# Kernel optimization log

Hardware: AMD Instinct MI355X
Metric: run time of the kernel (lower is better)

Reference implementation:

```python
import jax, jax.numpy as jnp
import numpy as np

B, S, IN, EMB, H = 4, 2048, 256, 512, 8
D = EMB // H
SCALE = 1.0 / np.sqrt(EMB)  # source uses 1/sqrt(embed_size), not head_dim
EPS = 1e-5


def setup_inputs() -> dict:
    key = jax.random.key(0)
    ks = jax.random.split(key, 20)
    def w(k, shape, fan_in):
        return jax.random.normal(k, shape, jnp.float32) * (1.0 / np.sqrt(fan_in))
    inp = {"state_emb": jax.random.normal(ks[0], (B, S, IN), jnp.float32)}
    i = 1
    for p in ("q", "k", "v"):
        inp[f"{p}_W1"] = w(ks[i], (IN, EMB), IN); i += 1
        inp[f"{p}_b1"] = jnp.zeros((EMB,), jnp.float32)
        inp[f"{p}_W2"] = w(ks[i], (EMB, EMB), EMB); i += 1
        inp[f"{p}_b2"] = jnp.zeros((EMB,), jnp.float32)
    inp["f_W1"] = w(ks[i], (EMB, 2 * EMB), EMB); i += 1
    inp["f_b1"] = jnp.zeros((2 * EMB,), jnp.float32)
    inp["f_W2"] = w(ks[i], (2 * EMB, EMB), 2 * EMB); i += 1
    inp["f_b2"] = jnp.zeros((EMB,), jnp.float32)
    inp["ln1_g"] = jnp.ones((EMB,), jnp.float32)
    inp["ln1_b"] = jnp.zeros((EMB,), jnp.float32)
    inp["ln2_g"] = jnp.ones((EMB,), jnp.float32)
    inp["ln2_b"] = jnp.zeros((EMB,), jnp.float32)
    return inp


def _mlp2(x, W1, b1, W2, b2):
    return jax.nn.relu(x @ W1 + b1) @ W2 + b2


def _layernorm(x, g, b):
    mu = jnp.mean(x, axis=-1, keepdims=True)
    var = jnp.mean(jnp.square(x - mu), axis=-1, keepdims=True)
    return (x - mu) * jax.lax.rsqrt(var + EPS) * g + b


def reference(state_emb, q_W1, q_b1, q_W2, q_b2, k_W1, k_b1, k_W2, k_b2,
              v_W1, v_b1, v_W2, v_b2, f_W1, f_b1, f_W2, f_b2,
              ln1_g, ln1_b, ln2_g, ln2_b):
    n, dim = state_emb.shape[0], state_emb.shape[1]
    q = _mlp2(state_emb, q_W1, q_b1, q_W2, q_b2)  # [n, dim, EMB]
    k = _mlp2(state_emb, k_W1, k_b1, k_W2, k_b2)
    v = _mlp2(state_emb, v_W1, v_b1, v_W2, v_b2)
    qh = q.reshape(n, dim, H, D)
    kh = k.reshape(n, dim, H, D)
    vh = v.reshape(n, dim, H, D)
    energy = jnp.einsum('nqhd,nkhd->nhqk', qh, kh)  # [n, H, dim, dim]
    attn = jax.nn.softmax(energy * SCALE, axis=-1)
    ctx = jnp.einsum('nhql,nlhd->nqhd', attn, vh).reshape(n, dim, EMB)
    x = _layernorm(ctx + q, ln1_g, ln1_b)  # residual with queries, per source
    ff = _mlp2(x, f_W1, f_b1, f_W2, f_b2)
    return _layernorm(x + ff, ln2_g, ln2_b)
```

## Files before the change

kernel.cpp:

```cpp
#include <hip/hip_runtime.h>
#include <hip/hip_bf16.h>
#include <math.h>

#define BB   4
#define SS   2048
#define INF_ 256
#define EMB  512
#define NH   8
#define HD   64
#define NT   8192

typedef unsigned short u16;
typedef unsigned int   u32;
typedef __attribute__((ext_vector_type(8))) short bf16x8;
typedef __attribute__((ext_vector_type(8))) unsigned short u16x8;
typedef __attribute__((ext_vector_type(4))) float f32x4;

constexpr float C2  = 0.06375871607f;
constexpr float RB  = 0.005624549f;
constexpr float TB  = 1.00390625f;
constexpr float EPS = 1e-5f;

__device__ __forceinline__ u16 f2bf(float v) {
    __hip_bfloat16 h = __float2bfloat16(v);
    return *(u16*)&h;
}
__device__ __forceinline__ float bf2f(u16 u) {
    __hip_bfloat16 h = *(__hip_bfloat16*)&u;
    return __bfloat162float(h);
}
__device__ __forceinline__ u16 ftrunc_bf(float v) {
    return (u16)(__float_as_uint(v * TB) >> 16);
}
__device__ __forceinline__ f32x4 mfma16(bf16x8 a, bf16x8 b, f32x4 c) {
    return __builtin_amdgcn_mfma_f32_16x16x32_bf16(a, b, c, 0, 0, 0);
}
__device__ __forceinline__ void async16(const void* g, void* l) {
    __builtin_amdgcn_global_load_lds(
        (const __attribute__((address_space(1))) void*)g,
        (__attribute__((address_space(3))) void*)l, 16, 0, 0);
}
__device__ __forceinline__ int derive_flag(const u16* x) {
    const int lane = threadIdx.x & 63;
    const unsigned e = (x[lane * 2] >> 7) & 0xFF;
    float pl = (e == 0 || (e >= 110 && e <= 140)) ? 1.0f : 0.0f;
    #pragma unroll
    for (int o = 1; o < 64; o <<= 1) pl += __shfl_xor(pl, o);
    return pl < 32.0f;
}

__global__ __launch_bounds__(256) void prep(
    const u16* __restrict__ xsrc,
    const void* w0, const void* w1, const void* w2, const void* w3,
    const void* w4, const void* w5, const void* w6, const void* w7,
    const void* p0, const void* p1, const void* p2, const void* p3,
    const void* p4, const void* p5, const void* p6, const void* p7,
    const void* p8, const void* p9, const void* p10, const void* p11,
    u16* __restrict__ xbf, u16* __restrict__ wt1, u16* __restrict__ wt2,
    u16* __restrict__ f1t, u16* __restrict__ f2t, float* __restrict__ small)
{
    const int isf = derive_flag(xsrc);
    const int z = blockIdx.z;
    const int tid = threadIdx.x;

    if (z < 8) {
        int K, M; const void* src; u16* dst;
        switch (z) {
            case 0: K=256;  M=512;  src=w0; dst=wt1;             break;
            case 1: K=256;  M=512;  src=w1; dst=wt1+512*256;     break;
            case 2: K=256;  M=512;  src=w2; dst=wt1+2*512*256;   break;
            case 3: K=512;  M=512;  src=w3; dst=wt2;             break;
            case 4: K=512;  M=512;  src=w4; dst=wt2+512*512;     break;
            case 5: K=512;  M=512;  src=w5; dst=wt2+2*512*512;   break;
            case 6: K=512;  M=1024; src=w6; dst=f1t;             break;
            default:K=1024; M=512;  src=w7; dst=f2t;             break;
        }
        const int m0 = blockIdx.x * 32, k0 = blockIdx.y * 32;
        if (m0 >= M || k0 >= K) return;
        __shared__ u16 t[32][33];
        const int tx = tid & 31, ty = tid >> 5;
        #pragma unroll
        for (int i = 0; i < 4; ++i) {
            const int kk = k0 + ty + i * 8;
            t[ty + i * 8][tx] = isf ? ftrunc_bf(((const float*)src)[(size_t)kk * M + m0 + tx])
                                    : ((const u16*)src)[(size_t)kk * M + m0 + tx];
        }
        __syncthreads();
        #pragma unroll
        for (int i = 0; i < 4; ++i) {
            const int mm = m0 + ty + i * 8;
            dst[(size_t)mm * K + k0 + tx] = t[tx][ty + i * 8];
        }
    } else if (z == 8) {
        const int bid = blockIdx.y * 32 + blockIdx.x;
        const int base = bid * 2048 + tid * 8;
        if (isf) {
            #pragma unroll
            for (int j = 0; j < 8; ++j)
                xbf[base + j] = ftrunc_bf(((const float*)xsrc)[base + j]);
        } else {
            *(u16x8*)&xbf[base] = *(const u16x8*)&xsrc[base];
        }
    } else {
        const int bid = blockIdx.y * 32 + blockIdx.x;
        if (bid >= 28) return;
        const int e = bid * 256 + tid;
        int id, i;
        if (e < 3072)      { id = e >> 9;               i = e & 511;          }
        else if (e < 4096) { id = 6;                    i = e - 3072;         }
        else               { id = 7 + ((e - 4096) >> 9); i = (e - 4096) & 511; }
        const void* src;
        switch (id) {
            case 0: src = p0; break;  case 1: src = p1; break;
            case 2: src = p2; break;  case 3: src = p3; break;
            case 4: src = p4; break;  case 5: src = p5; break;
            case 6: src = p6; break;  case 7: src = p7; break;
            case 8: src = p8; break;  case 9: src = p9; break;
            case 10: src = p10; break; default: src = p11; break;
        }
        small[e] = isf ? ((const float*)src)[i] : bf2f(((const u16*)src)[i]);
    }
}

template <int TR, int TC, bool RELU, bool AWHICH, bool VOUT>
__global__ __launch_bounds__(256) void gemm_bt(
    const u16* __restrict__ Aall, const u16* __restrict__ Wtall,
    const float* __restrict__ ball, u16* __restrict__ out,
    u16* __restrict__ vtb, int N, int K, int M)
{
    constexpr int RT = TR / 32, CT = TC / 32;
    constexpr int AR = TR / 32, BR = TC / 32;
    constexpr int SSTAGE = (TR + TC) * 64;
    constexpr int SELEMS = VOUT ? (SSTAGE > 128 * 136 ? SSTAGE : 128 * 136) : SSTAGE;
    __shared__ __align__(16) u16 smem[SELEMS];
    u16* sA = smem;
    u16* sB = smem + TR * 64;

    const int mtiles = M / TC;
    const int which = blockIdx.x / mtiles;
    const int colb  = blockIdx.x % mtiles;
    const int row0 = blockIdx.y * TR, col0 = colb * TC;
    const u16* A  = Aall + (AWHICH ? (size_t)which * N * K : 0);
    const u16* Wt = Wtall + (size_t)which * M * K;
    const float* bias = ball + (size_t)which * M;

    const int tid = threadIdx.x;
    const int lane = tid & 63, w = tid >> 6;
    const int wrow = (w & 1) * (TR / 2), wcol = (w >> 1) * (TC / 2);
    const int c = lane & 15, quad = lane >> 4;

    const u16* ap[AR]; const u16* bp[BR];
    #pragma unroll
    for (int i = 0; i < AR; ++i) {
        const int raw = i * 256 + tid, r = raw >> 3, ch = (raw & 7) ^ (r & 7);
        ap[i] = A + (size_t)(row0 + r) * K + ch * 8;
    }
    #pragma unroll
    for (int i = 0; i < BR; ++i) {
        const int raw = i * 256 + tid, r = raw >> 3, ch = (raw & 7) ^ (r & 7);
        bp[i] = Wt + (size_t)(col0 + r) * K + ch * 8;
    }

    f32x4 acc[RT][CT] = {};

    for (int k0 = 0; k0 < K; k0 += 64) {
        __syncthreads();
        #pragma unroll
        for (int i = 0; i < AR; ++i) {
            async16(ap[i], (char*)sA + (i * 256 + tid) * 16);
            ap[i] += 64;
        }
        #pragma unroll
        for (int i = 0; i < BR; ++i) {
            async16(bp[i], (char*)sB + (i * 256 + tid) * 16);
            bp[i] += 64;
        }
        __syncthreads();

        #pragma unroll
        for (int kt = 0; kt < 2; ++kt) {
            bf16x8 af[RT], bfr[CT];
            #pragma unroll
            for (int rt = 0; rt < RT; ++rt) {
                const int r = wrow + rt * 16 + c;
                af[rt] = *(const bf16x8*)&sA[(r * 8 + ((kt * 4 + quad) ^ (r & 7))) * 8];
            }
            #pragma unroll
            for (int ct = 0; ct < CT; ++ct) {
                const int r = wcol + ct * 16 + c;
                bfr[ct] = *(const bf16x8*)&sB[(r * 8 + ((kt * 4 + quad) ^ (r & 7))) * 8];
            }
            #pragma unroll
            for (int rt = 0; rt < RT; ++rt)
                #pragma unroll
                for (int ct = 0; ct < CT; ++ct)
                    acc[rt][ct] = mfma16(af[rt], bfr[ct], acc[rt][ct]);
        }
    }

    if (VOUT && which == 2) {
        __syncthreads();
        #pragma unroll
        for (int rt = 0; rt < RT; ++rt) {
            const int rowb = wrow + rt * 16 + quad * 4;
            #pragma unroll
            for (int ct = 0; ct < CT; ++ct) {
                const int col = wcol + ct * 16 + c;
                ushort4 pk;
                pk.x = ftrunc_bf(acc[rt][ct][0] + bias[col0 + col]);
                pk.y = ftrunc_bf(acc[rt][ct][1] + bias[col0 + col]);
                pk.z = ftrunc_bf(acc[rt][ct][2] + bias[col0 + col]);
                pk.w = ftrunc_bf(acc[rt][ct][3] + bias[col0 + col]);
                *(ushort4*)&smem[col * 136 + rowb] = pk;
            }
        }
        __syncthreads();
        const int dl = tid >> 1, half = tid & 1;
        const int hg = (col0 + dl) >> 6, dd = (col0 + dl) & 63;
        const int bb = row0 >> 11, s0 = row0 & 2047;
        u16* dst = vtb + ((size_t)(bb * NH + hg) * HD + dd) * SS + s0 + half * 64;
        #pragma unroll
        for (int j = 0; j < 8; ++j)
            *(u16x8*)&dst[j * 8] = *(const u16x8*)&smem[dl * 136 + half * 64 + j * 8];
        return;
    }

    const size_t outW = (size_t)which * N * M;
    #pragma unroll
    for (int rt = 0; rt < RT; ++rt) {
        #pragma unroll
        for (int i = 0; i < 4; ++i) {
            const int row = row0 + wrow + rt * 16 + quad * 4 + i;
            #pragma unroll
            for (int ct = 0; ct < CT; ++ct) {
                const int col = col0 + wcol + ct * 16 + c;
                float v = acc[rt][ct][i] + bias[col];
                if (RELU) v = fmaxf(v, 0.0f);
                out[outW + (size_t)row * M + col] = ftrunc_bf(v);
            }
        }
    }
}

__global__ __launch_bounds__(256) void attn_mfma(
    const u16* __restrict__ q, const u16* __restrict__ k,
    const u16* __restrict__ vt, u16* __restrict__ ctx)
{
    __shared__ __align__(16) u16 sK[2][64 * 64];
    __shared__ __align__(16) u16 sV[2][64 * 64];
    __shared__ __align__(16) u16 sP[4][32 * 64];

    const int tid = threadIdx.x;
    const int w = tid >> 6, lane = tid & 63;
    const int c = lane & 15, quad = lane >> 4;
    const int id = blockIdx.x;
    const int slot = id >> 3;
    const int bh = ((id & 7) << 2) | (slot >> 4);
    const int qt = slot & 15;
    const int b = bh >> 3, h = bh & 7;
    const int q0 = qt * 128;
    const size_t tokbase = (size_t)b * SS;
    const int hoff = h * HD;

    bf16x8 qf[2][2];
    #pragma unroll
    for (int f = 0; f < 2; ++f)
        #pragma unroll
        for (int kt = 0; kt < 2; ++kt)
            qf[f][kt] = *(const bf16x8*)&q[(tokbase + q0 + w * 32 + f * 16 + c) * EMB
                                           + hoff + kt * 32 + quad * 8];

    const u16* kp[2]; const u16* vp[2];
    #pragma unroll
    for (int i = 0; i < 2; ++i) {
        const int raw = i * 256 + tid, rr = raw >> 3, ch = (raw & 7) ^ (rr & 7);
        kp[i] = k + (tokbase + rr) * EMB + hoff + ch * 8;
        vp[i] = vt + ((size_t)(b * NH + h) * HD + rr) * SS + ch * 8;
    }
    auto stage = [&](int buf) {
        #pragma unroll
        for (int i = 0; i < 2; ++i) {
            async16(kp[i], (char*)sK[buf] + (i * 256 + tid) * 16);
            kp[i] += 64 * EMB;
        }
        #pragma unroll
        for (int i = 0; i < 2; ++i) {
            async16(vp[i], (char*)sV[buf] + (i * 256 + tid) * 16);
            vp[i] += 64;
        }
    };
    stage(0);

    float l0 = 0.0f, l1 = 0.0f;
    f32x4 accO[2][4] = {};

    for (int t = 0; t < SS / 64; ++t) {
        __syncthreads();
        const int buf = t & 1;
        if (t < SS / 64 - 1) stage(buf ^ 1);

        f32x4 accS[2][4] = {};
        #pragma unroll
        for (int mt = 0; mt < 4; ++mt) {
            const int key = mt * 16 + c;
            #pragma unroll
            for (int kt = 0; kt < 2; ++kt) {
                bf16x8 kf = *(const bf16x8*)&sK[buf][(key * 8 + ((kt * 4 + quad) ^ (key & 7))) * 8];
                accS[0][mt] = mfma16(kf, qf[0][kt], accS[0][mt]);
                accS[1][mt] = mfma16(kf, qf[1][kt], accS[1][mt]);
            }
        }

        #pragma unroll
        for (int f = 0; f < 2; ++f) {
            const int row = f * 16 + c;
            float ls = 0.0f;
            u32 pw[8];
            #pragma unroll
            for (int mt = 0; mt < 4; ++mt) {
                const float e0 = __builtin_amdgcn_exp2f(fmaf(accS[f][mt][0], C2, RB));
                const float e1 = __builtin_amdgcn_exp2f(fmaf(accS[f][mt][1], C2, RB));
                const float e2 = __builtin_amdgcn_exp2f(fmaf(accS[f][mt][2], C2, RB));
                const float e3 = __builtin_amdgcn_exp2f(fmaf(accS[f][mt][3], C2, RB));
                ls += (e0 + e1) + (e2 + e3);
                pw[2 * mt]     = __builtin_amdgcn_perm(__float_as_uint(e1), __float_as_uint(e0), 0x07060302u);
                pw[2 * mt + 1] = __builtin_amdgcn_perm(__float_as_uint(e3), __float_as_uint(e2), 0x07060302u);
            }
            if (f == 0) l0 += ls; else l1 += ls;
            #pragma unroll
            for (int mt = 0; mt < 4; ++mt) {
                const int chunk = 2 * mt + (quad >> 1);
                uint2 u; u.x = pw[2 * mt]; u.y = pw[2 * mt + 1];
                *(uint2*)((char*)&sP[w][0] + (row * 8 + (chunk ^ (c & 7))) * 16 + 8 * (quad & 1)) = u;
            }
        }

        bf16x8 pf[2][2];
        #pragma unroll
        for (int f = 0; f < 2; ++f)
            #pragma unroll
            for (int kt = 0; kt < 2; ++kt)
                pf[f][kt] = *(const bf16x8*)&sP[w][((f * 16 + c) * 8 + ((kt * 4 + quad) ^ (c & 7))) * 8];
        #pragma unroll
        for (int nt = 0; nt < 4; ++nt) {
            const int d = nt * 16 + c;
            #pragma unroll
            for (int kt = 0; kt < 2; ++kt) {
                bf16x8 vf = *(const bf16x8*)&sV[buf][(d * 8 + ((kt * 4 + quad) ^ (d & 7))) * 8];
                accO[0][nt] = mfma16(pf[0][kt], vf, accO[0][nt]);
                accO[1][nt] = mfma16(pf[1][kt], vf, accO[1][nt]);
            }
        }
    }

    #pragma unroll
    for (int f = 0; f < 2; ++f) {
        float l = (f == 0) ? l0 : l1;
        l += __shfl_xor(l, 16);
        l += __shfl_xor(l, 32);
        float li[4];
        #pragma unroll
        for (int i = 0; i < 4; ++i) {
            const float lv = __shfl(l, quad * 4 + i, 16);
            li[i] = (lv > 0.0f) ? (1.0f / lv) : 0.0f;
        }
        #pragma unroll
        for (int nt = 0; nt < 4; ++nt)
            #pragma unroll
            for (int i = 0; i < 4; ++i) {
                const int tok = q0 + w * 32 + f * 16 + quad * 4 + i;
                ctx[(tokbase + tok) * EMB + hoff + nt * 16 + c] =
                    ftrunc_bf(accO[f][nt][i] * li[i]);
            }
    }
}

__global__ __launch_bounds__(256) void ln_mid(
    const u16* __restrict__ a, const u16* __restrict__ b2,
    const float* __restrict__ g, const float* __restrict__ be,
    u16* __restrict__ outb)
{
    const int wave = threadIdx.x >> 6, lane = threadIdx.x & 63;
    const size_t row = (size_t)blockIdx.x * 4 + wave;
    const u16x8 av = *(const u16x8*)&a[row * EMB + lane * 8];
    const u16x8 bv = *(const u16x8*)&b2[row * EMB + lane * 8];
    float vals[8], sum = 0.0f;
    #pragma unroll
    for (int i = 0; i < 8; ++i) { vals[i] = bf2f(av[i]) + bf2f(bv[i]); sum += vals[i]; }
    #pragma unroll
    for (int o = 1; o < 64; o <<= 1) sum += __shfl_xor(sum, o);
    const float mu = sum * (1.0f / 512.0f);
    float vs = 0.0f;
    #pragma unroll
    for (int i = 0; i < 8; ++i) { const float d = vals[i] - mu; vs += d * d; }
    #pragma unroll
    for (int o = 1; o < 64; o <<= 1) vs += __shfl_xor(vs, o);
    const float rstd = rsqrtf(vs * (1.0f / 512.0f) + EPS);
    u16x8 ov;
    #pragma unroll
    for (int i = 0; i < 8; ++i) {
        const int col = lane * 8 + i;
        ov[i] = f2bf((vals[i] - mu) * rstd * g[col] + be[col]);
    }
    *(u16x8*)&outb[row * EMB + lane * 8] = ov;
}

__global__ __launch_bounds__(256) void ln_final(
    const u16* __restrict__ a, const u16* __restrict__ b2,
    const float* __restrict__ g, const float* __restrict__ be,
    void* __restrict__ dout, const u16* __restrict__ xsrc)
{
    const int isf = derive_flag(xsrc);
    const int wave = threadIdx.x >> 6, lane = threadIdx.x & 63;
    const size_t row = (size_t)blockIdx.x * 4 + wave;
    const u16x8 av = *(const u16x8*)&a[row * EMB + lane * 8];
    const u16x8 bv = *(const u16x8*)&b2[row * EMB + lane * 8];
    float vals[8], sum = 0.0f;
    #pragma unroll
    for (int i = 0; i < 8; ++i) { vals[i] = bf2f(av[i]) + bf2f(bv[i]); sum += vals[i]; }
    #pragma unroll
    for (int o = 1; o < 64; o <<= 1) sum += __shfl_xor(sum, o);
    const float mu = sum * (1.0f / 512.0f);
    float vs = 0.0f;
    #pragma unroll
    for (int i = 0; i < 8; ++i) { const float d = vals[i] - mu; vs += d * d; }
    #pragma unroll
    for (int o = 1; o < 64; o <<= 1) vs += __shfl_xor(vs, o);
    const float rstd = rsqrtf(vs * (1.0f / 512.0f) + EPS);
    if (isf) {
        #pragma unroll
        for (int i = 0; i < 8; ++i) {
            const int col = lane * 8 + i;
            ((float*)dout)[row * EMB + col] = (vals[i] - mu) * rstd * g[col] + be[col];
        }
    } else {
        u16x8 ov;
        #pragma unroll
        for (int i = 0; i < 8; ++i) {
            const int col = lane * 8 + i;
            ov[i] = f2bf((vals[i] - mu) * rstd * g[col] + be[col]);
        }
        *(u16x8*)&((u16*)dout)[row * EMB + lane * 8] = ov;
    }
}

extern "C" void kernel_launch(void* const* d_in, const int* in_sizes, int n_in,
                              void* d_out, int out_size, void* d_ws, size_t ws_size,
                              hipStream_t stream)
{
    char* ws = (char*)d_ws;
    float* small = (float*)(ws + 0);
    u16*   wt1   = (u16*)(ws + 32768);
    u16*   wt2   = (u16*)(ws + 819200);
    u16*   f1t   = (u16*)(ws + 2392064);
    u16*   f2t   = (u16*)(ws + 3440640);
    u16*   xbf   = (u16*)(ws + 4489216);
    u16*   h3    = (u16*)(ws + 8683520);
    u16*   qkv   = (u16*)(ws + 33849344);
    u16*   vtb   = (u16*)(ws + 59015168);
    u16*   ctxb  = (u16*)(ws + 67403776);
    u16*   x1b   = (u16*)(ws + 75792384);
    u16*   ffb   = (u16*)(ws + 84180992);

    const dim3 blk(256);
    const u16* xsrc = (const u16*)d_in[0];

    prep<<<dim3(32, 32, 10), blk, 0, stream>>>(
        xsrc,
        d_in[1], d_in[5], d_in[9], d_in[3], d_in[7], d_in[11], d_in[13], d_in[15],
        d_in[2], d_in[6], d_in[10], d_in[4], d_in[8], d_in[12],
        d_in[14], d_in[16], d_in[17], d_in[18], d_in[19], d_in[20],
        xbf, wt1, wt2, f1t, f2t, small);

    gemm_bt<128, 128, true, false, false><<<dim3(12, 64), blk, 0, stream>>>(
        xbf, wt1, small + 0, h3, nullptr, NT, INF_, EMB);
    gemm_bt<128, 128, false, true, true><<<dim3(12, 64), blk, 0, stream>>>(
        h3, wt2, small + 1536, qkv, vtb, NT, EMB, EMB);

    attn_mfma<<<dim3(512), blk, 0, stream>>>(
        qkv, qkv + (size_t)NT * EMB, vtb, ctxb);

    ln_mid<<<NT / 4, blk, 0, stream>>>(ctxb, qkv, small + 4608, small + 5120, x1b);

    u16* h2 = h3;
    gemm_bt<128, 128, true, false, false><<<dim3(8, 64), blk, 0, stream>>>(
        x1b, f1t, small + 3072, h2, nullptr, NT, EMB, 1024);
    gemm_bt<128, 64, false, false, false><<<dim3(8, 64), blk, 0, stream>>>(
        h2, f2t, small + 4096, ffb, nullptr, NT, 1024, EMB);

    ln_final<<<NT / 4, blk, 0, stream>>>(x1b, ffb, small + 5632, small + 6144, d_out, xsrc);
}
```

Baseline: 260.6 us.

## Double-buffer GEMM tiles, shrink attention query tile, pass P via bpermute

The GEMM kernel now double-buffers its A/B shared-memory tiles. It prefetches the next K-slice with async copies while computing the current one, which removes one barrier per iteration. The attention kernel drops to 64 queries per block (16 per wave) and is launched on twice as many blocks. Probabilities move from the S MFMA output layout to the PV operand layout with ds_bpermute instead of a shared-memory round trip. The QKV and FFN1 GEMMs switch to 128x64 tiles with twice the grid, trading some reuse for occupancy and parallelism.

```diff
diff --git a/kernel.cpp b/kernel.cpp
--- a/kernel.cpp
+++ b/kernel.cpp
@@ -130,11 +130,8 @@
 {
     constexpr int RT = TR / 32, CT = TC / 32;
     constexpr int AR = TR / 32, BR = TC / 32;
-    constexpr int SSTAGE = (TR + TC) * 64;
-    constexpr int SELEMS = VOUT ? (SSTAGE > 128 * 136 ? SSTAGE : 128 * 136) : SSTAGE;
-    __shared__ __align__(16) u16 smem[SELEMS];
-    u16* sA = smem;
-    u16* sB = smem + TR * 64;
+    __shared__ __align__(16) u16 sA[2][TR * 64];
+    __shared__ __align__(16) u16 sB[2][TC * 64];
 
     const int mtiles = M / TC;
     const int which = blockIdx.x / mtiles;
@@ -160,22 +157,27 @@
         const int raw = i * 256 + tid, r = raw >> 3, ch = (raw & 7) ^ (r & 7);
         bp[i] = Wt + (size_t)(col0 + r) * K + ch * 8;
     }
+    auto stage = [&](int buf) {
+        #pragma unroll
+        for (int i = 0; i < AR; ++i) {
+            async16(ap[i], (char*)&sA[buf][0] + (i * 256 + tid) * 16);
+            ap[i] += 64;
+        }
+        #pragma unroll
+        for (int i = 0; i < BR; ++i) {
+            async16(bp[i], (char*)&sB[buf][0] + (i * 256 + tid) * 16);
+            bp[i] += 64;
+        }
+    };
+    stage(0);
 
     f32x4 acc[RT][CT] = {};
-
-    for (int k0 = 0; k0 < K; k0 += 64) {
+    const int nIter = K >> 6;
+
+    for (int t = 0; t < nIter; ++t) {
         __syncthreads();
-        #pragma unroll
-        for (int i = 0; i < AR; ++i) {
-            async16(ap[i], (char*)sA + (i * 256 + tid) * 16);
-            ap[i] += 64;
-        }
-        #pragma unroll
-        for (int i = 0; i < BR; ++i) {
-            async16(bp[i], (char*)sB + (i * 256 + tid) * 16);
-            bp[i] += 64;
-        }
-        __syncthreads();
+        const int buf = t & 1;
+        if (t + 1 < nIter) stage(buf ^ 1);
 
         #pragma unroll
         for (int kt = 0; kt < 2; ++kt) {
@@ -183,12 +185,12 @@
             #pragma unroll
             for (int rt = 0; rt < RT; ++rt) {
                 const int r = wrow + rt * 16 + c;
-                af[rt] = *(const bf16x8*)&sA[(r * 8 + ((kt * 4 + quad) ^ (r & 7))) * 8];
+                af[rt] = *(const bf16x8*)&sA[buf][(r * 8 + ((kt * 4 + quad) ^ (r & 7))) * 8];
             }
             #pragma unroll
             for (int ct = 0; ct < CT; ++ct) {
                 const int r = wcol + ct * 16 + c;
-                bfr[ct] = *(const bf16x8*)&sB[(r * 8 + ((kt * 4 + quad) ^ (r & 7))) * 8];
+                bfr[ct] = *(const bf16x8*)&sB[buf][(r * 8 + ((kt * 4 + quad) ^ (r & 7))) * 8];
             }
             #pragma unroll
             for (int rt = 0; rt < RT; ++rt)
@@ -199,6 +201,7 @@
     }
 
     if (VOUT && which == 2) {
+        u16* smem = &sA[0][0];
         __syncthreads();
         #pragma unroll
         for (int rt = 0; rt < RT; ++rt) {
@@ -206,22 +209,23 @@
             #pragma unroll
             for (int ct = 0; ct < CT; ++ct) {
                 const int col = wcol + ct * 16 + c;
+                const float bb = bias[col0 + col];
                 ushort4 pk;
-                pk.x = ftrunc_bf(acc[rt][ct][0] + bias[col0 + col]);
-                pk.y = ftrunc_bf(acc[rt][ct][1] + bias[col0 + col]);
-                pk.z = ftrunc_bf(acc[rt][ct][2] + bias[col0 + col]);
-                pk.w = ftrunc_bf(acc[rt][ct][3] + bias[col0 + col]);
+                pk.x = ftrunc_bf(acc[rt][ct][0] + bb);
+                pk.y = ftrunc_bf(acc[rt][ct][1] + bb);
+                pk.z = ftrunc_bf(acc[rt][ct][2] + bb);
+                pk.w = ftrunc_bf(acc[rt][ct][3] + bb);
                 *(ushort4*)&smem[col * 136 + rowb] = pk;
             }
         }
         __syncthreads();
-        const int dl = tid >> 1, half = tid & 1;
-        const int hg = (col0 + dl) >> 6, dd = (col0 + dl) & 63;
+        const int dcol = tid >> 2, part = tid & 3;
+        const int hg = (col0 + dcol) >> 6, dd = (col0 + dcol) & 63;
         const int bb = row0 >> 11, s0 = row0 & 2047;
-        u16* dst = vtb + ((size_t)(bb * NH + hg) * HD + dd) * SS + s0 + half * 64;
-        #pragma unroll
-        for (int j = 0; j < 8; ++j)
-            *(u16x8*)&dst[j * 8] = *(const u16x8*)&smem[dl * 136 + half * 64 + j * 8];
+        u16* dst = vtb + ((size_t)(bb * NH + hg) * HD + dd) * SS + s0 + part * 32;
+        #pragma unroll
+        for (int j = 0; j < 4; ++j)
+            *(u16x8*)&dst[j * 8] = *(const u16x8*)&smem[dcol * 136 + part * 32 + j * 8];
         return;
     }
 
@@ -248,27 +252,24 @@
 {
     __shared__ __align__(16) u16 sK[2][64 * 64];
     __shared__ __align__(16) u16 sV[2][64 * 64];
-    __shared__ __align__(16) u16 sP[4][32 * 64];
 
     const int tid = threadIdx.x;
     const int w = tid >> 6, lane = tid & 63;
     const int c = lane & 15, quad = lane >> 4;
     const int id = blockIdx.x;
     const int slot = id >> 3;
-    const int bh = ((id & 7) << 2) | (slot >> 4);
-    const int qt = slot & 15;
+    const int bh = ((id & 7) << 2) | (slot >> 5);
+    const int qt = slot & 31;
     const int b = bh >> 3, h = bh & 7;
-    const int q0 = qt * 128;
+    const int q0 = qt * 64;
     const size_t tokbase = (size_t)b * SS;
     const int hoff = h * HD;
 
-    bf16x8 qf[2][2];
-    #pragma unroll
-    for (int f = 0; f < 2; ++f)
-        #pragma unroll
-        for (int kt = 0; kt < 2; ++kt)
-            qf[f][kt] = *(const bf16x8*)&q[(tokbase + q0 + w * 32 + f * 16 + c) * EMB
-                                           + hoff + kt * 32 + quad * 8];
+    const int myq = q0 + w * 16 + c;
+    bf16x8 qf[2];
+    #pragma unroll
+    for (int kt = 0; kt < 2; ++kt)
+        qf[kt] = *(const bf16x8*)&q[(tokbase + myq) * EMB + hoff + kt * 32 + quad * 8];
 
     const u16* kp[2]; const u16* vp[2];
     #pragma unroll
@@ -280,98 +281,85 @@
     auto stage = [&](int buf) {
         #pragma unroll
         for (int i = 0; i < 2; ++i) {
-            async16(kp[i], (char*)sK[buf] + (i * 256 + tid) * 16);
+            async16(kp[i], (char*)&sK[buf][0] + (i * 256 + tid) * 16);
             kp[i] += 64 * EMB;
         }
         #pragma unroll
         for (int i = 0; i < 2; ++i) {
-            async16(vp[i], (char*)sV[buf] + (i * 256 + tid) * 16);
+            async16(vp[i], (char*)&sV[buf][0] + (i * 256 + tid) * 16);
             vp[i] += 64;
         }
     };
     stage(0);
 
-    float l0 = 0.0f, l1 = 0.0f;
-    f32x4 accO[2][4] = {};
+    const int addr0 = (c + 16 * ((quad & 1) * 2)) * 4;
+    const int addr1 = addr0 + 64;
+
+    float l_lane = 0.0f;
+    f32x4 accO[4] = {};
 
     for (int t = 0; t < SS / 64; ++t) {
         __syncthreads();
         const int buf = t & 1;
-        if (t < SS / 64 - 1) stage(buf ^ 1);
-
-        f32x4 accS[2][4] = {};
+        if (t + 1 < SS / 64) stage(buf ^ 1);
+
+        f32x4 accS[4] = {};
         #pragma unroll
         for (int mt = 0; mt < 4; ++mt) {
             const int key = mt * 16 + c;
             #pragma unroll
             for (int kt = 0; kt < 2; ++kt) {
                 bf16x8 kf = *(const bf16x8*)&sK[buf][(key * 8 + ((kt * 4 + quad) ^ (key & 7))) * 8];
-                accS[0][mt] = mfma16(kf, qf[0][kt], accS[0][mt]);
-                accS[1][mt] = mfma16(kf, qf[1][kt], accS[1][mt]);
-            }
-        }
-
-        #pragma unroll
-        for (int f = 0; f < 2; ++f) {
-            const int row = f * 16 + c;
-            float ls = 0.0f;
-            u32 pw[8];
-            #pragma unroll
-            for (int mt = 0; mt < 4; ++mt) {
-                const float e0 = __builtin_amdgcn_exp2f(fmaf(accS[f][mt][0], C2, RB));
-                const float e1 = __builtin_amdgcn_exp2f(fmaf(accS[f][mt][1], C2, RB));
-                const float e2 = __builtin_amdgcn_exp2f(fmaf(accS[f][mt][2], C2, RB));
-                const float e3 = __builtin_amdgcn_exp2f(fmaf(accS[f][mt][3], C2, RB));
-                ls += (e0 + e1) + (e2 + e3);
-                pw[2 * mt]     = __builtin_amdgcn_perm(__float_as_uint(e1), __float_as_uint(e0), 0x07060302u);
-                pw[2 * mt + 1] = __builtin_amdgcn_perm(__float_as_uint(e3), __float_as_uint(e2), 0x07060302u);
-            }
-            if (f == 0) l0 += ls; else l1 += ls;
-            #pragma unroll
-            for (int mt = 0; mt < 4; ++mt) {
-                const int chunk = 2 * mt + (quad >> 1);
-                uint2 u; u.x = pw[2 * mt]; u.y = pw[2 * mt + 1];
-                *(uint2*)((char*)&sP[w][0] + (row * 8 + (chunk ^ (c & 7))) * 16 + 8 * (quad & 1)) = u;
-            }
-        }
-
-        bf16x8 pf[2][2];
-        #pragma unroll
-        for (int f = 0; f < 2; ++f)
-            #pragma unroll
-            for (int kt = 0; kt < 2; ++kt)
-                pf[f][kt] = *(const bf16x8*)&sP[w][((f * 16 + c) * 8 + ((kt * 4 + quad) ^ (c & 7))) * 8];
-        #pragma unroll
-        for (int nt = 0; nt < 4; ++nt) {
-            const int d = nt * 16 + c;
-            #pragma unroll
-            for (int kt = 0; kt < 2; ++kt) {
+                accS[mt] = mfma16(kf, qf[kt], accS[mt]);
+            }
+        }
+
+        u32 pw[8];
+        float ls = 0.0f;
+        #pragma unroll
+        for (int mt = 0; mt < 4; ++mt) {
+            const float e0 = __builtin_amdgcn_exp2f(fmaf(accS[mt][0], C2, RB));
+            const float e1 = __builtin_amdgcn_exp2f(fmaf(accS[mt][1], C2, RB));
+            const float e2 = __builtin_amdgcn_exp2f(fmaf(accS[mt][2], C2, RB));
+            const float e3 = __builtin_amdgcn_exp2f(fmaf(accS[mt][3], C2, RB));
+            ls += (e0 + e1) + (e2 + e3);
+            pw[2 * mt]     = __builtin_amdgcn_perm(__float_as_uint(e1), __float_as_uint(e0), 0x07060302u);
+            pw[2 * mt + 1] = __builtin_amdgcn_perm(__float_as_uint(e3), __float_as_uint(e2), 0x07060302u);
+        }
+        l_lane += ls;
+
+        #pragma unroll
+        for (int kt = 0; kt < 2; ++kt) {
+            const int m = (quad >> 1) + 2 * kt;
+            union { u32 u[4]; bf16x8 v; } pb;
+            pb.u[0] = (u32)__builtin_amdgcn_ds_bpermute(addr0, (int)pw[2 * m]);
+            pb.u[1] = (u32)__builtin_amdgcn_ds_bpermute(addr0, (int)pw[2 * m + 1]);
+            pb.u[2] = (u32)__builtin_amdgcn_ds_bpermute(addr1, (int)pw[2 * m]);
+            pb.u[3] = (u32)__builtin_amdgcn_ds_bpermute(addr1, (int)pw[2 * m + 1]);
+            #pragma unroll
+            for (int nt = 0; nt < 4; ++nt) {
+                const int d = nt * 16 + c;
                 bf16x8 vf = *(const bf16x8*)&sV[buf][(d * 8 + ((kt * 4 + quad) ^ (d & 7))) * 8];
-                accO[0][nt] = mfma16(pf[0][kt], vf, accO[0][nt]);
-                accO[1][nt] = mfma16(pf[1][kt], vf, accO[1][nt]);
-            }
-        }
-    }
-
-    #pragma unroll
-    for (int f = 0; f < 2; ++f) {
-        float l = (f == 0) ? l0 : l1;
-        l += __shfl_xor(l, 16);
-        l += __shfl_xor(l, 32);
-        float li[4];
-        #pragma unroll
-        for (int i = 0; i < 4; ++i) {
-            const float lv = __shfl(l, quad * 4 + i, 16);
-            li[i] = (lv > 0.0f) ? (1.0f / lv) : 0.0f;
-        }
-        #pragma unroll
-        for (int nt = 0; nt < 4; ++nt)
-            #pragma unroll
-            for (int i = 0; i < 4; ++i) {
-                const int tok = q0 + w * 32 + f * 16 + quad * 4 + i;
-                ctx[(tokbase + tok) * EMB + hoff + nt * 16 + c] =
-                    ftrunc_bf(accO[f][nt][i] * li[i]);
-            }
+                accO[nt] = mfma16(vf, pb.v, accO[nt]);
+            }
+        }
+    }
+
+    float l = l_lane;
+    l += __shfl_xor(l, 16);
+    l += __shfl_xor(l, 32);
+    const float li = (l > 0.0f) ? (1.0f / l) : 0.0f;
+
+    const int tok = q0 + w * 16 + c;
+    u16* dst = ctx + (tokbase + tok) * EMB + hoff + quad * 4;
+    #pragma unroll
+    for (int nt = 0; nt < 4; ++nt) {
+        ushort4 pk;
+        pk.x = ftrunc_bf(accO[nt][0] * li);
+        pk.y = ftrunc_bf(accO[nt][1] * li);
+        pk.z = ftrunc_bf(accO[nt][2] * li);
+        pk.w = ftrunc_bf(accO[nt][3] * li);
+        *(ushort4*)&dst[nt * 16] = pk;
     }
 }
 
@@ -472,18 +460,18 @@
         d_in[14], d_in[16], d_in[17], d_in[18], d_in[19], d_in[20],
         xbf, wt1, wt2, f1t, f2t, small);
 
-    gemm_bt<128, 128, true, false, false><<<dim3(12, 64), blk, 0, stream>>>(
+    gemm_bt<128, 64, true, false, false><<<dim3(24, 64), blk, 0, stream>>>(
         xbf, wt1, small + 0, h3, nullptr, NT, INF_, EMB);
-    gemm_bt<128, 128, false, true, true><<<dim3(12, 64), blk, 0, stream>>>(
+    gemm_bt<128, 64, false, true, true><<<dim3(24, 64), blk, 0, stream>>>(
         h3, wt2, small + 1536, qkv, vtb, NT, EMB, EMB);
 
-    attn_mfma<<<dim3(512), blk, 0, stream>>>(
+    attn_mfma<<<dim3(1024), blk, 0, stream>>>(
         qkv, qkv + (size_t)NT * EMB, vtb, ctxb);
 
     ln_mid<<<NT / 4, blk, 0, stream>>>(ctxb, qkv, small + 4608, small + 5120, x1b);
 
     u16* h2 = h3;
-    gemm_bt<128, 128, true, false, false><<<dim3(8, 64), blk, 0, stream>>>(
+    gemm_bt<128, 64, true, false, false><<<dim3(16, 64), blk, 0, stream>>>(
         x1b, f1t, small + 3072, h2, nullptr, NT, EMB, 1024);
     gemm_bt<128, 64, false, false, false><<<dim3(8, 64), blk, 0, stream>>>(
         h2, f2t, small + 4096, ffb, nullptr, NT, 1024, EMB);
```

New measurement: 273.5 us. 5.0% more time.
